# Kernel optimization log

Hardware: AMD Instinct MI355X
Metric: run time of the kernel (lower is better)

Reference implementation:

```python
import jax, jax.numpy as jnp
import numpy as np

B, N, DIM = 2, 2048, 1024
HEADS = 16
DIM_HEAD = DIM // HEADS  # 64
SCALE = DIM_HEAD ** -0.5


def setup_inputs() -> dict:
    key = jax.random.key(0)
    k1, k2, k3 = jax.random.split(key, 3)
    x = jax.random.normal(k1, (B, N, DIM), dtype=jnp.float32)
    W_qkv = jax.random.normal(k2, (DIM, 3 * HEADS * DIM_HEAD), dtype=jnp.float32) * (DIM ** -0.5)
    W_out = jax.random.normal(k3, (HEADS * DIM_HEAD, DIM), dtype=jnp.float32) * (DIM ** -0.5)
    return {"x": x, "W_qkv": W_qkv, "W_out": W_out}


def reference(x, W_qkv, W_out):
    b, n, _ = x.shape
    qkv = jnp.einsum('bnd,de->bne', x, W_qkv)  # [b, n, 3*h*dh]
    # faithful to einops 'b n (d k h) -> k b h n d': last axis factored as (dh, 3, h)
    qkv = qkv.reshape(b, n, DIM_HEAD, 3, HEADS)
    qkv = jnp.transpose(qkv, (3, 0, 4, 1, 2))  # [3, b, h, n, dh]
    q, k, v = qkv[0], qkv[1], qkv[2]
    scores = jnp.einsum('bhid,bhjd->bhij', q, k) * SCALE  # [b, h, n, n]
    causal_mask = jnp.triu(jnp.ones((n, n), dtype=bool), k=1)
    scores = jnp.where(causal_mask, -jnp.inf, scores)
    attn = jax.nn.softmax(scores, axis=-1)
    out = jnp.einsum('bhij,bhjd->bhid', attn, v)  # [b, h, n, dh]
    out = jnp.transpose(out, (0, 2, 1, 3)).reshape(b, n, HEADS * DIM_HEAD)  # 'b h n d -> b n (h d)'
    return jnp.einsum('bne,ed->bnd', out, W_out)
```

## Files before the change

kernel.cpp:

```cpp
#include <hip/hip_runtime.h>

typedef _Float16 f16;
typedef f16 half8 __attribute__((ext_vector_type(8)));
typedef f16 f16x4 __attribute__((ext_vector_type(4)));
typedef float f32x4 __attribute__((ext_vector_type(4)));

#define GLOAD_LDS16(gsrc, ldst)                                                              \
  __builtin_amdgcn_global_load_lds((const __attribute__((address_space(1))) void*)(gsrc),    \
                                   (__attribute__((address_space(3))) void*)(ldst), 16, 0, 0)

constexpr float SCALE = 0.125f;

__global__ __launch_bounds__(256) void k_cvt(const float4* __restrict__ in,
                                             f16x4* __restrict__ out, int n4) {
  int i = blockIdx.x * 256 + threadIdx.x;
  if (i < n4) {
    float4 v = in[i];
    f16x4 o;
    o[0] = (f16)v.x; o[1] = (f16)v.y; o[2] = (f16)v.z; o[3] = (f16)v.w;
    out[i] = o;
  }
}

__global__ __launch_bounds__(256) void k_transpose(const float* __restrict__ in,
                                                   f16* __restrict__ out, int R, int C) {
  __shared__ float t[32][33];
  int c0 = blockIdx.x * 32, r0 = blockIdx.y * 32;
  int tx = threadIdx.x, ty = threadIdx.y;
  for (int i = ty; i < 32; i += 8) t[i][tx] = in[(size_t)(r0 + i) * C + c0 + tx];
  __syncthreads();
  for (int i = ty; i < 32; i += 8) out[(size_t)(c0 + i) * R + r0 + tx] = (f16)t[tx][i];
}

__global__ __launch_bounds__(256) void k_transpose_qkv(const float* __restrict__ in,
                                                       f16* __restrict__ out) {
  __shared__ float t[32][33];
  int c0 = blockIdx.x * 32, r0 = blockIdx.y * 32;
  int tx = threadIdx.x, ty = threadIdx.y;
  for (int i = ty; i < 32; i += 8) t[i][tx] = in[(size_t)(r0 + i) * 3072 + c0 + tx];
  __syncthreads();
  for (int i = ty; i < 32; i += 8) {
    const int e = c0 + i;
    const int d = e / 48, rem = e - d * 48;
    const int k = rem >> 4, h = rem & 15;
    const int ep = k * 1024 + h * 64 + d;
    out[(size_t)ep * 1024 + r0 + tx] = (f16)t[tx][i];
  }
}

template <int MODE>
__global__ __launch_bounds__(256) void k_gemm(const f16* __restrict__ A,
                                              const f16* __restrict__ Bt,
                                              float* __restrict__ C,
                                              f16* __restrict__ Qp,
                                              f16* __restrict__ Kp,
                                              f16* __restrict__ Vt) {
  constexpr int K = 1024, BK = 64;
  __shared__ alignas(16) f16 smem[128 * 128];
  f16* As = smem;
  f16* Bs = smem + 128 * 64;
  const int tid = threadIdx.x;
  const int w = tid >> 6, lane = tid & 63;
  const int g = lane >> 4, lr = lane & 15;
  const int wr = w >> 1, wc = w & 1;
  const int m0 = blockIdx.y * 128, n0 = blockIdx.x * 128;
  const int srow = lane >> 3;
  const int scol = ((lane & 7) ^ srow) << 3;

  f32x4 acc[4][4] = {};

  for (int kt = 0; kt < K; kt += BK) {
    __syncthreads();
#pragma unroll
    for (int i = 0; i < 4; ++i) {
      const int chunk = w * 4 + i;
      const int row = chunk * 8 + srow;
      GLOAD_LDS16(A + (size_t)(m0 + row) * K + kt + scol, &As[chunk * 512]);
      GLOAD_LDS16(Bt + (size_t)(n0 + row) * K + kt + scol, &Bs[chunk * 512]);
    }
    __syncthreads();
#pragma unroll
    for (int c = 0; c < 2; ++c) {
      half8 af[4], bf[4];
#pragma unroll
      for (int m = 0; m < 4; ++m) {
        const int ra = wr * 64 + m * 16 + lr;
        const int off = ra * 128 + ((((c << 2) | g) ^ (ra & 7)) << 4);
        af[m] = *(const half8*)((const char*)As + off);
      }
#pragma unroll
      for (int n = 0; n < 4; ++n) {
        const int rb = wc * 64 + n * 16 + lr;
        const int off = rb * 128 + ((((c << 2) | g) ^ (rb & 7)) << 4);
        bf[n] = *(const half8*)((const char*)Bs + off);
      }
#pragma unroll
      for (int m = 0; m < 4; ++m)
#pragma unroll
        for (int n = 0; n < 4; ++n)
          acc[m][n] = __builtin_amdgcn_mfma_f32_16x16x32_f16(af[m], bf[n], acc[m][n], 0, 0, 0);
    }
  }

  if constexpr (MODE == 0) {
    const int sec = n0 >> 10;
    const int base = n0 & 1023;
    const int b = m0 >> 11;
    if (sec < 2) {
      f16* __restrict__ dst = (sec == 0) ? Qp : Kp;
      const float mul = (sec == 0) ? SCALE : 1.0f;
#pragma unroll
      for (int n = 0; n < 4; ++n) {
        const int idx = base + wc * 64 + n * 16 + lr;
        const int h = idx >> 6, d = idx & 63;
        f16* __restrict__ dh = dst + ((size_t)(b * 16 + h) * 2048) * 64 + d;
#pragma unroll
        for (int m = 0; m < 4; ++m)
#pragma unroll
          for (int r = 0; r < 4; ++r) {
            const int nn = (m0 & 2047) + wr * 64 + m * 16 + 4 * g + r;
            dh[(size_t)nn * 64] = (f16)(acc[m][n][r] * mul);
          }
      }
    } else {
      char* sb = (char*)smem;
      __syncthreads();
#pragma unroll
      for (int m = 0; m < 4; ++m)
#pragma unroll
        for (int n = 0; n < 4; ++n) {
          const int col = wc * 64 + n * 16 + lr;
          const int tok0 = wr * 64 + m * 16 + 4 * g;
          f16x4 v4;
#pragma unroll
          for (int r = 0; r < 4; ++r) v4[r] = (f16)acc[m][n][r];
          *(f16x4*)(sb + col * 256 + ((tok0 * 2) ^ ((col & 15) << 4))) = v4;
        }
      __syncthreads();
      const int nn0 = m0 & 2047;
#pragma unroll
      for (int pass = 0; pass < 8; ++pass) {
        const int c = w * 32 + pass * 4 + g;
        const int idx = base + c;
        const int h = idx >> 6, d = idx & 63;
        const half8 v = *(const half8*)(sb + c * 256 + ((lr * 16) ^ ((c & 15) << 4)));
        *(half8*)(Vt + ((size_t)(b * 16 + h) * 64 + d) * 2048 + nn0 + lr * 8) = v;
      }
    }
  } else {
#pragma unroll
    for (int m = 0; m < 4; ++m)
#pragma unroll
      for (int n = 0; n < 4; ++n)
#pragma unroll
        for (int r = 0; r < 4; ++r)
          C[(size_t)(m0 + wr * 64 + m * 16 + 4 * g + r) * 1024 +
            (n0 + wc * 64 + n * 16 + lr)] = acc[m][n][r];
  }
}

__global__ __launch_bounds__(256, 2) void k_attn(const f16* __restrict__ Q,
                                                 const f16* __restrict__ Kp,
                                                 const f16* __restrict__ Vt,
                                                 f16* __restrict__ O) {
  __shared__ alignas(16) f16 plds_all[4][2][16][72];
  const int tid = threadIdx.x;
  const int w = tid >> 6, lane = tid & 63;
  const int g = lane >> 4, lr = lane & 15;
  const int bh = blockIdx.x & 31;
  const int u = blockIdx.x >> 5;
  const int t = (u < 8) ? u : 23 - u;
  const int q0 = t * 128 + w * 32;
  f16(*plds)[16][72] = plds_all[w];

  const f16* __restrict__ Qb = Q + (size_t)bh * (2048 * 64);
  const f16* __restrict__ Kb = Kp + (size_t)bh * (2048 * 64);
  const f16* __restrict__ Vb = Vt + (size_t)bh * (64 * 2048);

  half8 qf[2][2];
#pragma unroll
  for (int f = 0; f < 2; ++f)
#pragma unroll
    for (int c = 0; c < 2; ++c)
      qf[f][c] = *(const half8*)(Qb + (size_t)(q0 + 16 * f + lr) * 64 + 32 * c + 8 * g);

  f32x4 acc[2][4] = {};
  float mrow[2][4], lrow[2][4];
#pragma unroll
  for (int f = 0; f < 2; ++f)
#pragma unroll
    for (int r = 0; r < 4; ++r) {
      mrow[f][r] = -INFINITY;
      lrow[f][r] = 0.f;
    }

  const int ntiles = (q0 + 31) / 64 + 1;

  half8 kc[4][2], kn[4][2];
#pragma unroll
  for (int j = 0; j < 4; ++j)
#pragma unroll
    for (int c = 0; c < 2; ++c)
      kc[j][c] = *(const half8*)(Kb + (size_t)(16 * j + lr) * 64 + 32 * c + 8 * g);

  for (int kt = 0; kt < ntiles; ++kt) {
    const int k0 = kt * 64;
    half8 va[4][2];
#pragma unroll
    for (int nb = 0; nb < 4; ++nb)
#pragma unroll
      for (int c = 0; c < 2; ++c)
        va[nb][c] = *(const half8*)(Vb + (size_t)(16 * nb + lr) * 2048 + k0 + 32 * c + 8 * g);
    const int knext = (kt + 1 < ntiles ? kt + 1 : kt) * 64;
#pragma unroll
    for (int j = 0; j < 4; ++j)
#pragma unroll
      for (int c = 0; c < 2; ++c)
        kn[j][c] = *(const half8*)(Kb + (size_t)(knext + 16 * j + lr) * 64 + 32 * c + 8 * g);

    f32x4 s[2][4];
#pragma unroll
    for (int f = 0; f < 2; ++f)
#pragma unroll
      for (int j = 0; j < 4; ++j) {
        f32x4 z = {};
        z = __builtin_amdgcn_mfma_f32_16x16x32_f16(qf[f][0], kc[j][0], z, 0, 0, 0);
        s[f][j] = __builtin_amdgcn_mfma_f32_16x16x32_f16(qf[f][1], kc[j][1], z, 0, 0, 0);
      }

    if (k0 + 63 > q0) {
#pragma unroll
      for (int f = 0; f < 2; ++f)
#pragma unroll
        for (int j = 0; j < 4; ++j) {
          const int key = k0 + 16 * j + lr;
#pragma unroll
          for (int r = 0; r < 4; ++r)
            if (key > q0 + 16 * f + 4 * g + r) s[f][j][r] = -INFINITY;
        }
    }

#pragma unroll
    for (int f = 0; f < 2; ++f)
#pragma unroll
      for (int r = 0; r < 4; ++r) {
        float tmax = fmaxf(fmaxf(s[f][0][r], s[f][1][r]), fmaxf(s[f][2][r], s[f][3][r]));
        tmax = fmaxf(tmax, __shfl_xor(tmax, 1));
        tmax = fmaxf(tmax, __shfl_xor(tmax, 2));
        tmax = fmaxf(tmax, __shfl_xor(tmax, 4));
        tmax = fmaxf(tmax, __shfl_xor(tmax, 8));
        const float mn = fmaxf(mrow[f][r], tmax);
        const float sf = __expf(mrow[f][r] - mn);
        mrow[f][r] = mn;
        float rs = 0.f;
#pragma unroll
        for (int j = 0; j < 4; ++j) {
          const float pv = __expf(s[f][j][r] - mn);
          s[f][j][r] = pv;
          rs += pv;
        }
        rs += __shfl_xor(rs, 1);
        rs += __shfl_xor(rs, 2);
        rs += __shfl_xor(rs, 4);
        rs += __shfl_xor(rs, 8);
        lrow[f][r] = lrow[f][r] * sf + rs;
#pragma unroll
        for (int nb = 0; nb < 4; ++nb) acc[f][nb][r] *= sf;
      }

#pragma unroll
    for (int f = 0; f < 2; ++f)
#pragma unroll
      for (int j = 0; j < 4; ++j)
#pragma unroll
        for (int r = 0; r < 4; ++r)
          plds[f][4 * g + r][16 * j + lr] = (f16)s[f][j][r];
    asm volatile("s_waitcnt lgkmcnt(0)" ::: "memory");
    __builtin_amdgcn_sched_barrier(0);
    half8 pf[2][2];
#pragma unroll
    for (int f = 0; f < 2; ++f)
#pragma unroll
      for (int c = 0; c < 2; ++c)
        pf[f][c] = *(const half8*)(&plds[f][lr][32 * c + 8 * g]);

#pragma unroll
    for (int f = 0; f < 2; ++f)
#pragma unroll
      for (int nb = 0; nb < 4; ++nb) {
        acc[f][nb] = __builtin_amdgcn_mfma_f32_16x16x32_f16(pf[f][0], va[nb][0], acc[f][nb], 0, 0, 0);
        acc[f][nb] = __builtin_amdgcn_mfma_f32_16x16x32_f16(pf[f][1], va[nb][1], acc[f][nb], 0, 0, 0);
      }
    __builtin_amdgcn_sched_barrier(0);

#pragma unroll
    for (int j = 0; j < 4; ++j)
#pragma unroll
      for (int c = 0; c < 2; ++c)
        kc[j][c] = kn[j][c];
  }

  const int b = bh >> 4, h = bh & 15;
#pragma unroll
  for (int f = 0; f < 2; ++f)
#pragma unroll
    for (int r = 0; r < 4; ++r) {
      const float inv = 1.f / lrow[f][r];
      const int q = q0 + 16 * f + 4 * g + r;
      f16* orow = O + ((size_t)(b * 2048 + q) * 1024) + h * 64;
#pragma unroll
      for (int nb = 0; nb < 4; ++nb) orow[16 * nb + lr] = (f16)(acc[f][nb][r] * inv);
    }
}

extern "C" void kernel_launch(void* const* d_in, const int* in_sizes, int n_in,
                              void* d_out, int out_size, void* d_ws, size_t ws_size,
                              hipStream_t stream) {
  const float* x = (const float*)d_in[0];
  const float* Wqkv = (const float*)d_in[1];
  const float* Wout = (const float*)d_in[2];

  char* p = (char*)d_ws;
  f16* Xb = (f16*)p;    p += (size_t)4096 * 1024 * 2;
  f16* Wqkvt = (f16*)p; p += (size_t)3072 * 1024 * 2;
  f16* Woutt = (f16*)p; p += (size_t)1024 * 1024 * 2;
  f16* Qp = (f16*)p;    p += (size_t)32 * 2048 * 64 * 2;
  f16* Kp = (f16*)p;    p += (size_t)32 * 2048 * 64 * 2;
  f16* Vt = (f16*)p;    p += (size_t)32 * 64 * 2048 * 2;
  f16* O = (f16*)p;     p += (size_t)4096 * 1024 * 2;

  k_cvt<<<4096, 256, 0, stream>>>((const float4*)x, (f16x4*)Xb, 4096 * 1024 / 4);
  k_transpose_qkv<<<dim3(96, 32), dim3(32, 8), 0, stream>>>(Wqkv, Wqkvt);
  k_transpose<<<dim3(32, 32), dim3(32, 8), 0, stream>>>(Wout, Woutt, 1024, 1024);
  k_gemm<0><<<dim3(24, 32), 256, 0, stream>>>(Xb, Wqkvt, nullptr, Qp, Kp, Vt);
  k_attn<<<512, 256, 0, stream>>>(Qp, Kp, Vt, O);
  k_gemm<1><<<dim3(8, 32), 256, 0, stream>>>(O, Woutt, (float*)d_out, nullptr, nullptr, nullptr);
}
```

Baseline: 221.8 us.

## Use single-wave attention blocks with transposed S tile and exp2 softmax

Turns the attention kernel into 64-thread single-wave blocks, one per 32-query strip. Blocks are ordered heaviest-first and interleaved across a modulo-8 mapping for causal load balance. It computes S transposed (K as the A operand) so each lane holds one query row and row reductions need only two cross-lane shuffles. It also folds log2(e) into the Q scaling so softmax uses exp2, and adds s_setprio around the MFMA phases. Risks include lower occupancy limits per block and extra shuffles to broadcast rescale factors to the PV accumulator layout.

Result: slower. 252.2 us (+13.7%).

```diff
diff --git a/kernel.cpp b/kernel.cpp
--- a/kernel.cpp
+++ b/kernel.cpp
@@ -10,6 +10,14 @@
                                    (__attribute__((address_space(3))) void*)(ldst), 16, 0, 0)
 
 constexpr float SCALE = 0.125f;
+constexpr float SCALE_L2E = 0.125f * 1.4426950408889634f;
+
+static __device__ __forceinline__ f32x4 vmax4(f32x4 a, f32x4 b) {
+  f32x4 r;
+  r[0] = fmaxf(a[0], b[0]); r[1] = fmaxf(a[1], b[1]);
+  r[2] = fmaxf(a[2], b[2]); r[3] = fmaxf(a[3], b[3]);
+  return r;
+}
 
 __global__ __launch_bounds__(256) void k_cvt(const float4* __restrict__ in,
                                              f16x4* __restrict__ out, int n4) {
@@ -108,7 +116,7 @@
     const int b = m0 >> 11;
     if (sec < 2) {
       f16* __restrict__ dst = (sec == 0) ? Qp : Kp;
-      const float mul = (sec == 0) ? SCALE : 1.0f;
+      const float mul = (sec == 0) ? SCALE_L2E : 1.0f;
 #pragma unroll
       for (int n = 0; n < 4; ++n) {
         const int idx = base + wc * 64 + n * 16 + lr;
@@ -159,19 +167,17 @@
   }
 }
 
-__global__ __launch_bounds__(256, 2) void k_attn(const f16* __restrict__ Q,
-                                                 const f16* __restrict__ Kp,
-                                                 const f16* __restrict__ Vt,
-                                                 f16* __restrict__ O) {
-  __shared__ alignas(16) f16 plds_all[4][2][16][72];
-  const int tid = threadIdx.x;
-  const int w = tid >> 6, lane = tid & 63;
+__global__ __launch_bounds__(64, 3) void k_attn(const f16* __restrict__ Q,
+                                                const f16* __restrict__ Kp,
+                                                const f16* __restrict__ Vt,
+                                                f16* __restrict__ O) {
+  __shared__ alignas(16) f16 plds[2][16][72];
+  const int lane = threadIdx.x;
   const int g = lane >> 4, lr = lane & 15;
-  const int bh = blockIdx.x & 31;
-  const int u = blockIdx.x >> 5;
-  const int t = (u < 8) ? u : 23 - u;
-  const int q0 = t * 128 + w * 32;
-  f16(*plds)[16][72] = plds_all[w];
+  const int id = (blockIdx.x & 7) * 256 + (blockIdx.x >> 3);
+  const int bh = id >> 6;
+  const int t = 63 - (id & 63);
+  const int q0 = t * 32;
 
   const f16* __restrict__ Qb = Q + (size_t)bh * (2048 * 64);
   const f16* __restrict__ Kb = Kp + (size_t)bh * (2048 * 64);
@@ -185,16 +191,10 @@
       qf[f][c] = *(const half8*)(Qb + (size_t)(q0 + 16 * f + lr) * 64 + 32 * c + 8 * g);
 
   f32x4 acc[2][4] = {};
-  float mrow[2][4], lrow[2][4];
-#pragma unroll
-  for (int f = 0; f < 2; ++f)
-#pragma unroll
-    for (int r = 0; r < 4; ++r) {
-      mrow[f][r] = -INFINITY;
-      lrow[f][r] = 0.f;
-    }
-
-  const int ntiles = (q0 + 31) / 64 + 1;
+  float mrow[2] = {-INFINITY, -INFINITY};
+  float lrow[2] = {0.f, 0.f};
+
+  const int ntiles = (q0 >> 6) + 1;
 
   half8 kc[4][2], kn[4][2];
 #pragma unroll
@@ -205,76 +205,83 @@
 
   for (int kt = 0; kt < ntiles; ++kt) {
     const int k0 = kt * 64;
+    const int knext = (kt + 1 < ntiles ? kt + 1 : kt) * 64;
+#pragma unroll
+    for (int j = 0; j < 4; ++j)
+#pragma unroll
+      for (int c = 0; c < 2; ++c)
+        kn[j][c] = *(const half8*)(Kb + (size_t)(knext + 16 * j + lr) * 64 + 32 * c + 8 * g);
+
+    __builtin_amdgcn_s_setprio(1);
+    f32x4 st[2][4];
+#pragma unroll
+    for (int f = 0; f < 2; ++f)
+#pragma unroll
+      for (int j = 0; j < 4; ++j) {
+        f32x4 z = {};
+        z = __builtin_amdgcn_mfma_f32_16x16x32_f16(kc[j][0], qf[f][0], z, 0, 0, 0);
+        st[f][j] = __builtin_amdgcn_mfma_f32_16x16x32_f16(kc[j][1], qf[f][1], z, 0, 0, 0);
+      }
+    __builtin_amdgcn_s_setprio(0);
+
     half8 va[4][2];
 #pragma unroll
     for (int nb = 0; nb < 4; ++nb)
 #pragma unroll
       for (int c = 0; c < 2; ++c)
         va[nb][c] = *(const half8*)(Vb + (size_t)(16 * nb + lr) * 2048 + k0 + 32 * c + 8 * g);
-    const int knext = (kt + 1 < ntiles ? kt + 1 : kt) * 64;
-#pragma unroll
-    for (int j = 0; j < 4; ++j)
-#pragma unroll
-      for (int c = 0; c < 2; ++c)
-        kn[j][c] = *(const half8*)(Kb + (size_t)(knext + 16 * j + lr) * 64 + 32 * c + 8 * g);
-
-    f32x4 s[2][4];
+
+    if (k0 + 63 > q0) {
+#pragma unroll
+      for (int f = 0; f < 2; ++f)
+#pragma unroll
+        for (int j = 0; j < 4; ++j) {
+          const int keyb = k0 + 16 * j + 4 * g;
+          const int q = q0 + 16 * f + lr;
+#pragma unroll
+          for (int r = 0; r < 4; ++r)
+            if (keyb + r > q) st[f][j][r] = -INFINITY;
+        }
+    }
+
+    float sfv[2];
+#pragma unroll
+    for (int f = 0; f < 2; ++f) {
+      f32x4 m4 = vmax4(vmax4(st[f][0], st[f][1]), vmax4(st[f][2], st[f][3]));
+      float tm = fmaxf(fmaxf(m4[0], m4[1]), fmaxf(m4[2], m4[3]));
+      tm = fmaxf(tm, __shfl_xor(tm, 16));
+      tm = fmaxf(tm, __shfl_xor(tm, 32));
+      const float mn = fmaxf(mrow[f], tm);
+      sfv[f] = __builtin_amdgcn_exp2f(mrow[f] - mn);
+      mrow[f] = mn;
+#pragma unroll
+      for (int j = 0; j < 4; ++j)
+#pragma unroll
+        for (int r = 0; r < 4; ++r)
+          st[f][j][r] = __builtin_amdgcn_exp2f(st[f][j][r] - mn);
+      f32x4 s4 = st[f][0] + st[f][1] + st[f][2] + st[f][3];
+      float rs = (s4[0] + s4[1]) + (s4[2] + s4[3]);
+      rs += __shfl_xor(rs, 16);
+      rs += __shfl_xor(rs, 32);
+      lrow[f] = lrow[f] * sfv[f] + rs;
+#pragma unroll
+      for (int j = 0; j < 4; ++j) {
+        f16x4 v4;
+#pragma unroll
+        for (int r = 0; r < 4; ++r) v4[r] = (f16)st[f][j][r];
+        *(f16x4*)(&plds[f][lr][16 * j + 4 * g]) = v4;
+      }
+    }
+
 #pragma unroll
     for (int f = 0; f < 2; ++f)
 #pragma unroll
-      for (int j = 0; j < 4; ++j) {
-        f32x4 z = {};
-        z = __builtin_amdgcn_mfma_f32_16x16x32_f16(qf[f][0], kc[j][0], z, 0, 0, 0);
-        s[f][j] = __builtin_amdgcn_mfma_f32_16x16x32_f16(qf[f][1], kc[j][1], z, 0, 0, 0);
-      }
-
-    if (k0 + 63 > q0) {
-#pragma unroll
-      for (int f = 0; f < 2; ++f)
-#pragma unroll
-        for (int j = 0; j < 4; ++j) {
-          const int key = k0 + 16 * j + lr;
-#pragma unroll
-          for (int r = 0; r < 4; ++r)
-            if (key > q0 + 16 * f + 4 * g + r) s[f][j][r] = -INFINITY;
-        }
-    }
-
-#pragma unroll
-    for (int f = 0; f < 2; ++f)
-#pragma unroll
       for (int r = 0; r < 4; ++r) {
-        float tmax = fmaxf(fmaxf(s[f][0][r], s[f][1][r]), fmaxf(s[f][2][r], s[f][3][r]));
-        tmax = fmaxf(tmax, __shfl_xor(tmax, 1));
-        tmax = fmaxf(tmax, __shfl_xor(tmax, 2));
-        tmax = fmaxf(tmax, __shfl_xor(tmax, 4));
-        tmax = fmaxf(tmax, __shfl_xor(tmax, 8));
-        const float mn = fmaxf(mrow[f][r], tmax);
-        const float sf = __expf(mrow[f][r] - mn);
-        mrow[f][r] = mn;
-        float rs = 0.f;
-#pragma unroll
-        for (int j = 0; j < 4; ++j) {
-          const float pv = __expf(s[f][j][r] - mn);
-          s[f][j][r] = pv;
-          rs += pv;
-        }
-        rs += __shfl_xor(rs, 1);
-        rs += __shfl_xor(rs, 2);
-        rs += __shfl_xor(rs, 4);
-        rs += __shfl_xor(rs, 8);
-        lrow[f][r] = lrow[f][r] * sf + rs;
-#pragma unroll
-        for (int nb = 0; nb < 4; ++nb) acc[f][nb][r] *= sf;
-      }
-
-#pragma unroll
-    for (int f = 0; f < 2; ++f)
-#pragma unroll
-      for (int j = 0; j < 4; ++j)
-#pragma unroll
-        for (int r = 0; r < 4; ++r)
-          plds[f][4 * g + r][16 * j + lr] = (f16)s[f][j][r];
+        const float sb = __shfl(sfv[f], 4 * g + r);
+#pragma unroll
+        for (int nb = 0; nb < 4; ++nb) acc[f][nb][r] *= sb;
+      }
+
     asm volatile("s_waitcnt lgkmcnt(0)" ::: "memory");
     __builtin_amdgcn_sched_barrier(0);
     half8 pf[2][2];
@@ -284,6 +291,7 @@
       for (int c = 0; c < 2; ++c)
         pf[f][c] = *(const half8*)(&plds[f][lr][32 * c + 8 * g]);
 
+    __builtin_amdgcn_s_setprio(1);
 #pragma unroll
     for (int f = 0; f < 2; ++f)
 #pragma unroll
@@ -291,6 +299,7 @@
         acc[f][nb] = __builtin_amdgcn_mfma_f32_16x16x32_f16(pf[f][0], va[nb][0], acc[f][nb], 0, 0, 0);
         acc[f][nb] = __builtin_amdgcn_mfma_f32_16x16x32_f16(pf[f][1], va[nb][1], acc[f][nb], 0, 0, 0);
       }
+    __builtin_amdgcn_s_setprio(0);
     __builtin_amdgcn_sched_barrier(0);
 
 #pragma unroll
@@ -305,7 +314,8 @@
   for (int f = 0; f < 2; ++f)
 #pragma unroll
     for (int r = 0; r < 4; ++r) {
-      const float inv = 1.f / lrow[f][r];
+      const float lb = __shfl(lrow[f], 4 * g + r);
+      const float inv = 1.f / lb;
       const int q = q0 + 16 * f + 4 * g + r;
       f16* orow = O + ((size_t)(b * 2048 + q) * 1024) + h * 64;
 #pragma unroll
@@ -333,6 +343,6 @@
   k_transpose_qkv<<<dim3(96, 32), dim3(32, 8), 0, stream>>>(Wqkv, Wqkvt);
   k_transpose<<<dim3(32, 32), dim3(32, 8), 0, stream>>>(Wout, Woutt, 1024, 1024);
   k_gemm<0><<<dim3(24, 32), 256, 0, stream>>>(Xb, Wqkvt, nullptr, Qp, Kp, Vt);
-  k_attn<<<512, 256, 0, stream>>>(Qp, Kp, Vt, O);
+  k_attn<<<2048, 64, 0, stream>>>(Qp, Kp, Vt, O);
   k_gemm<1><<<dim3(8, 32), 256, 0, stream>>>(O, Woutt, (float*)d_out, nullptr, nullptr, nullptr);
 }
```

## Stage K/V tiles in shared LDS with double-buffered async loads; use exp2 softmax

Applied to the files above, without the earlier changes.

The attention kernel now loads each 64-key K and V tile once per workgroup into swizzled, double-buffered LDS using global_load_lds, so the four waves share it instead of each fetching K/V from global memory. The next tile is prefetched while the current one is computed, with workgroup barriers in between, and waves skip tiles entirely beyond their causal range. Q is prescaled by log2(e) in the projection epilogue so the softmax can use exp2 directly, and setprio is raised around the MFMA blocks. In exchange it adds two barriers per tile, makes every wave follow the longest wave's tile count, and uses extra LDS that may cut occupancy.

Result: slower. 230.3 us (+3.8%).

```diff
diff --git a/kernel.cpp b/kernel.cpp
--- a/kernel.cpp
+++ b/kernel.cpp
@@ -9,7 +9,15 @@
   __builtin_amdgcn_global_load_lds((const __attribute__((address_space(1))) void*)(gsrc),    \
                                    (__attribute__((address_space(3))) void*)(ldst), 16, 0, 0)
 
+#define WGBAR()                            \
+  do {                                     \
+    __builtin_amdgcn_sched_barrier(0);     \
+    __builtin_amdgcn_s_barrier();          \
+    __builtin_amdgcn_sched_barrier(0);     \
+  } while (0)
+
 constexpr float SCALE = 0.125f;
+constexpr float SCALE_L2E = 0.125f * 1.4426950408889634f;
 
 __global__ __launch_bounds__(256) void k_cvt(const float4* __restrict__ in,
                                              f16x4* __restrict__ out, int n4) {
@@ -108,7 +116,7 @@
     const int b = m0 >> 11;
     if (sec < 2) {
       f16* __restrict__ dst = (sec == 0) ? Qp : Kp;
-      const float mul = (sec == 0) ? SCALE : 1.0f;
+      const float mul = (sec == 0) ? SCALE_L2E : 1.0f;
 #pragma unroll
       for (int n = 0; n < 4; ++n) {
         const int idx = base + wc * 64 + n * 16 + lr;
@@ -163,6 +171,8 @@
                                                  const f16* __restrict__ Kp,
                                                  const f16* __restrict__ Vt,
                                                  f16* __restrict__ O) {
+  __shared__ alignas(16) f16 Ks[2][4096];
+  __shared__ alignas(16) f16 Vs[2][4096];
   __shared__ alignas(16) f16 plds_all[4][2][16][72];
   const int tid = threadIdx.x;
   const int w = tid >> 6, lane = tid & 63;
@@ -174,8 +184,8 @@
   f16(*plds)[16][72] = plds_all[w];
 
   const f16* __restrict__ Qb = Q + (size_t)bh * (2048 * 64);
-  const f16* __restrict__ Kb = Kp + (size_t)bh * (2048 * 64);
-  const f16* __restrict__ Vb = Vt + (size_t)bh * (64 * 2048);
+  const char* __restrict__ Kb = (const char*)(Kp + (size_t)bh * (2048 * 64));
+  const char* __restrict__ Vb = (const char*)(Vt + (size_t)bh * (64 * 2048));
 
   half8 qf[2][2];
 #pragma unroll
@@ -194,110 +204,134 @@
       lrow[f][r] = 0.f;
     }
 
-  const int ntiles = (q0 + 31) / 64 + 1;
-
-  half8 kc[4][2], kn[4][2];
-#pragma unroll
-  for (int j = 0; j < 4; ++j)
-#pragma unroll
-    for (int c = 0; c < 2; ++c)
-      kc[j][c] = *(const half8*)(Kb + (size_t)(16 * j + lr) * 64 + 32 * c + 8 * g);
-
-  for (int kt = 0; kt < ntiles; ++kt) {
+  const int nt = 2 * t + 2;
+  const int srow8 = lane >> 3;
+  const int sc = ((lane & 7) ^ srow8) << 4;
+
+  auto stage = [&](int k0s, int buf) {
+#pragma unroll
+    for (int p = 0; p < 2; ++p) {
+      const int o = (p * 4 + w) * 1024;
+      const int row = (p * 4 + w) * 8 + srow8;
+      GLOAD_LDS16(Kb + (size_t)(k0s + row) * 128 + sc, (char*)Ks[buf] + o);
+      GLOAD_LDS16(Vb + (size_t)row * 4096 + (size_t)k0s * 2 + sc, (char*)Vs[buf] + o);
+    }
+  };
+
+  stage(0, 0);
+  asm volatile("s_waitcnt vmcnt(0)" ::: "memory");
+  WGBAR();
+
+  for (int kt = 0; kt < nt; ++kt) {
     const int k0 = kt * 64;
-    half8 va[4][2];
-#pragma unroll
-    for (int nb = 0; nb < 4; ++nb)
-#pragma unroll
-      for (int c = 0; c < 2; ++c)
-        va[nb][c] = *(const half8*)(Vb + (size_t)(16 * nb + lr) * 2048 + k0 + 32 * c + 8 * g);
-    const int knext = (kt + 1 < ntiles ? kt + 1 : kt) * 64;
-#pragma unroll
-    for (int j = 0; j < 4; ++j)
-#pragma unroll
-      for (int c = 0; c < 2; ++c)
-        kn[j][c] = *(const half8*)(Kb + (size_t)(knext + 16 * j + lr) * 64 + 32 * c + 8 * g);
-
-    f32x4 s[2][4];
-#pragma unroll
-    for (int f = 0; f < 2; ++f)
-#pragma unroll
-      for (int j = 0; j < 4; ++j) {
-        f32x4 z = {};
-        z = __builtin_amdgcn_mfma_f32_16x16x32_f16(qf[f][0], kc[j][0], z, 0, 0, 0);
-        s[f][j] = __builtin_amdgcn_mfma_f32_16x16x32_f16(qf[f][1], kc[j][1], z, 0, 0, 0);
-      }
-
-    if (k0 + 63 > q0) {
+    const int buf = kt & 1;
+    if (kt + 1 < nt) {
+      stage(k0 + 64, buf ^ 1);
+      asm volatile("s_waitcnt vmcnt(4)" ::: "memory");
+    } else {
+      asm volatile("s_waitcnt vmcnt(0)" ::: "memory");
+    }
+    WGBAR();
+
+    if (k0 <= q0) {
+      half8 kf[4][2];
+#pragma unroll
+      for (int j = 0; j < 4; ++j)
+#pragma unroll
+        for (int c = 0; c < 2; ++c)
+          kf[j][c] = *(const half8*)((const char*)Ks[buf] + (16 * j + lr) * 128 +
+                                     ((64 * c + 16 * g) ^ ((lr & 7) << 4)));
+
+      __builtin_amdgcn_s_setprio(1);
+      f32x4 s[2][4];
 #pragma unroll
       for (int f = 0; f < 2; ++f)
 #pragma unroll
         for (int j = 0; j < 4; ++j) {
-          const int key = k0 + 16 * j + lr;
+          f32x4 z = {};
+          z = __builtin_amdgcn_mfma_f32_16x16x32_f16(qf[f][0], kf[j][0], z, 0, 0, 0);
+          s[f][j] = __builtin_amdgcn_mfma_f32_16x16x32_f16(qf[f][1], kf[j][1], z, 0, 0, 0);
+        }
+      __builtin_amdgcn_s_setprio(0);
+
+      half8 va[4][2];
+#pragma unroll
+      for (int nb = 0; nb < 4; ++nb)
+#pragma unroll
+        for (int c = 0; c < 2; ++c)
+          va[nb][c] = *(const half8*)((const char*)Vs[buf] + (16 * nb + lr) * 128 +
+                                      ((64 * c + 16 * g) ^ ((lr & 7) << 4)));
+
+      if (k0 + 63 > q0) {
+#pragma unroll
+        for (int f = 0; f < 2; ++f)
+#pragma unroll
+          for (int j = 0; j < 4; ++j) {
+            const int key = k0 + 16 * j + lr;
+#pragma unroll
+            for (int r = 0; r < 4; ++r)
+              if (key > q0 + 16 * f + 4 * g + r) s[f][j][r] = -INFINITY;
+          }
+      }
+
+#pragma unroll
+      for (int f = 0; f < 2; ++f)
+#pragma unroll
+        for (int r = 0; r < 4; ++r) {
+          float tmax = fmaxf(fmaxf(s[f][0][r], s[f][1][r]), fmaxf(s[f][2][r], s[f][3][r]));
+          tmax = fmaxf(tmax, __shfl_xor(tmax, 1));
+          tmax = fmaxf(tmax, __shfl_xor(tmax, 2));
+          tmax = fmaxf(tmax, __shfl_xor(tmax, 4));
+          tmax = fmaxf(tmax, __shfl_xor(tmax, 8));
+          const float mn = fmaxf(mrow[f][r], tmax);
+          const float sf = __builtin_amdgcn_exp2f(mrow[f][r] - mn);
+          mrow[f][r] = mn;
+          float rs = 0.f;
+#pragma unroll
+          for (int j = 0; j < 4; ++j) {
+            const float pv = __builtin_amdgcn_exp2f(s[f][j][r] - mn);
+            s[f][j][r] = pv;
+            rs += pv;
+          }
+          rs += __shfl_xor(rs, 1);
+          rs += __shfl_xor(rs, 2);
+          rs += __shfl_xor(rs, 4);
+          rs += __shfl_xor(rs, 8);
+          lrow[f][r] = lrow[f][r] * sf + rs;
+#pragma unroll
+          for (int nb = 0; nb < 4; ++nb) acc[f][nb][r] *= sf;
+        }
+
+#pragma unroll
+      for (int f = 0; f < 2; ++f)
+#pragma unroll
+        for (int j = 0; j < 4; ++j)
 #pragma unroll
           for (int r = 0; r < 4; ++r)
-            if (key > q0 + 16 * f + 4 * g + r) s[f][j][r] = -INFINITY;
+            plds[f][4 * g + r][16 * j + lr] = (f16)s[f][j][r];
+      asm volatile("s_waitcnt lgkmcnt(0)" ::: "memory");
+      __builtin_amdgcn_sched_barrier(0);
+      half8 pf[2][2];
+#pragma unroll
+      for (int f = 0; f < 2; ++f)
+#pragma unroll
+        for (int c = 0; c < 2; ++c)
+          pf[f][c] = *(const half8*)(&plds[f][lr][32 * c + 8 * g]);
+
+      __builtin_amdgcn_s_setprio(1);
+#pragma unroll
+      for (int f = 0; f < 2; ++f)
+#pragma unroll
+        for (int nb = 0; nb < 4; ++nb) {
+          acc[f][nb] =
+              __builtin_amdgcn_mfma_f32_16x16x32_f16(pf[f][0], va[nb][0], acc[f][nb], 0, 0, 0);
+          acc[f][nb] =
+              __builtin_amdgcn_mfma_f32_16x16x32_f16(pf[f][1], va[nb][1], acc[f][nb], 0, 0, 0);
         }
-    }
-
-#pragma unroll
-    for (int f = 0; f < 2; ++f)
-#pragma unroll
-      for (int r = 0; r < 4; ++r) {
-        float tmax = fmaxf(fmaxf(s[f][0][r], s[f][1][r]), fmaxf(s[f][2][r], s[f][3][r]));
-        tmax = fmaxf(tmax, __shfl_xor(tmax, 1));
-        tmax = fmaxf(tmax, __shfl_xor(tmax, 2));
-        tmax = fmaxf(tmax, __shfl_xor(tmax, 4));
-        tmax = fmaxf(tmax, __shfl_xor(tmax, 8));
-        const float mn = fmaxf(mrow[f][r], tmax);
-        const float sf = __expf(mrow[f][r] - mn);
-        mrow[f][r] = mn;
-        float rs = 0.f;
-#pragma unroll
-        for (int j = 0; j < 4; ++j) {
-          const float pv = __expf(s[f][j][r] - mn);
-          s[f][j][r] = pv;
-          rs += pv;
-        }
-        rs += __shfl_xor(rs, 1);
-        rs += __shfl_xor(rs, 2);
-        rs += __shfl_xor(rs, 4);
-        rs += __shfl_xor(rs, 8);
-        lrow[f][r] = lrow[f][r] * sf + rs;
-#pragma unroll
-        for (int nb = 0; nb < 4; ++nb) acc[f][nb][r] *= sf;
-      }
-
-#pragma unroll
-    for (int f = 0; f < 2; ++f)
-#pragma unroll
-      for (int j = 0; j < 4; ++j)
-#pragma unroll
-        for (int r = 0; r < 4; ++r)
-          plds[f][4 * g + r][16 * j + lr] = (f16)s[f][j][r];
-    asm volatile("s_waitcnt lgkmcnt(0)" ::: "memory");
-    __builtin_amdgcn_sched_barrier(0);
-    half8 pf[2][2];
-#pragma unroll
-    for (int f = 0; f < 2; ++f)
-#pragma unroll
-      for (int c = 0; c < 2; ++c)
-        pf[f][c] = *(const half8*)(&plds[f][lr][32 * c + 8 * g]);
-
-#pragma unroll
-    for (int f = 0; f < 2; ++f)
-#pragma unroll
-      for (int nb = 0; nb < 4; ++nb) {
-        acc[f][nb] = __builtin_amdgcn_mfma_f32_16x16x32_f16(pf[f][0], va[nb][0], acc[f][nb], 0, 0, 0);
-        acc[f][nb] = __builtin_amdgcn_mfma_f32_16x16x32_f16(pf[f][1], va[nb][1], acc[f][nb], 0, 0, 0);
-      }
-    __builtin_amdgcn_sched_barrier(0);
-
-#pragma unroll
-    for (int j = 0; j < 4; ++j)
-#pragma unroll
-      for (int c = 0; c < 2; ++c)
-        kc[j][c] = kn[j][c];
+      __builtin_amdgcn_s_setprio(0);
+    }
+
+    WGBAR();
   }
 
   const int b = bh >> 4, h = bh & 15;
```
